# Kernel optimization log

Hardware: AMD Instinct MI355X
Metric: run time of the kernel (lower is better)

The kernel has to match this reference:

```python
import jax, jax.numpy as jnp
import numpy as np

B, N, D, H, F = 16, 512, 768, 12, 3072
HD = D // H
EPS = 1e-5
NEG_INF = -1e30  # stand-in for -inf; softmax of all -inf rows handled via nan_to_num semantics


def layer_norm(x, g, b):
    mu = jnp.mean(x, axis=-1, keepdims=True)
    var = jnp.mean(jnp.square(x - mu), axis=-1, keepdims=True)
    return (x - mu) * jax.lax.rsqrt(var + EPS) * g + b


def setup_inputs() -> dict:
    key = jax.random.key(0)
    ks = jax.random.split(key, 16)
    s = 0.02
    return {
        "x": jax.random.normal(ks[0], (B, N, D), jnp.float32),
        "spatial_encoding": jax.random.normal(ks[1], (B, N, N), jnp.float32),
        "edge_encoding": jax.random.normal(ks[2], (B, N, N), jnp.float32),
        "Wq": jax.random.normal(ks[3], (D, D), jnp.float32) * s,
        "Wk": jax.random.normal(ks[4], (D, D), jnp.float32) * s,
        "Wv": jax.random.normal(ks[5], (D, D), jnp.float32) * s,
        "bv": jnp.zeros((D,), jnp.float32),
        "Wo": jax.random.normal(ks[6], (D, D), jnp.float32) * s,
        "bo": jnp.zeros((D,), jnp.float32),
        "g1": jnp.ones((D,), jnp.float32),
        "be1": jnp.zeros((D,), jnp.float32),
        "g2": jnp.ones((D,), jnp.float32),
        "be2": jnp.zeros((D,), jnp.float32),
        "W1": jax.random.normal(ks[7], (D, F), jnp.float32) * s,
        "bf1": jnp.zeros((F,), jnp.float32),
        "W2": jax.random.normal(ks[8], (F, D), jnp.float32) * s,
        "bf2": jnp.zeros((D,), jnp.float32),
    }


def reference(x, spatial_encoding, edge_encoding, Wq, Wk, Wv, bv, Wo, bo,
              g1, be1, g2, be2, W1, bf1, W2, bf2):
    scale = D ** (-0.5)
    h = layer_norm(x, g1, be1)                              # n1(x)
    bias = (spatial_encoding + edge_encoding)[:, None]      # [B,1,N,N]

    q = (h @ Wq).reshape(B, N, H, HD).transpose(0, 2, 1, 3)  # [B,H,N,hd]
    k = (h @ Wk).reshape(B, N, H, HD).transpose(0, 2, 1, 3)
    v = (h @ Wv + bv).reshape(B, N, H, HD).transpose(0, 2, 1, 3)

    a = jnp.einsum('bhqd,bhkd->bhqk', q, k) * scale + bias   # [B,H,N,N]
    # pad rows (all-zero score rows) get -inf -> softmax NaN -> nan_to_num -> 0
    row_nonzero = jnp.any(a != 0, axis=-1, keepdims=True)
    a = jnp.where(row_nonzero, a, NEG_INF)
    p = jax.nn.softmax(a, axis=-1)
    p = jnp.where(row_nonzero, p, 0.0)  # mirrors nan_to_num on all -inf rows

    o = jnp.einsum('bhqk,bhkd->bhqd', p, v)                  # [B,H,N,hd]
    o = o.transpose(0, 2, 1, 3).reshape(B, N, D)
    att_output = o @ Wo + bo + x                              # residual

    pad_mask = jnp.any(att_output == 0, axis=-1)              # [B,N]
    ffn_in = layer_norm(x, g2, be2)                           # note: n2(x), as in source
    hmid = jax.nn.gelu(ffn_in @ W1 + bf1, approximate=True)
    ffn_out = hmid @ W2 + bf2 + att_output
    return jnp.where(pad_mask[..., None], 0.0, ffn_out)
```

## Files before the change

kernel.cpp:

```cpp
#include <hip/hip_runtime.h>
#include <math.h>

typedef unsigned short u16;
typedef __bf16 bf16x8 __attribute__((ext_vector_type(8)));
typedef float f32x4 __attribute__((ext_vector_type(4)));

__device__ __forceinline__ u16 f2bf(float f){
  union{float f; unsigned u;} v; v.f = f;
  return (u16)((v.u + 0x7fffu + ((v.u >> 16) & 1u)) >> 16);
}

#define LOG2E 1.4426950408889634f

__global__ __launch_bounds__(256) void prep_all(
    const float* __restrict__ sp, const float* __restrict__ ed,
    const float* __restrict__ Wq, const float* __restrict__ Wk,
    const float* __restrict__ Wv, const float* __restrict__ Wo,
    const float* __restrict__ W1, const float* __restrict__ W2,
    const float* __restrict__ g1, const float* __restrict__ g2,
    const float* __restrict__ be1, const float* __restrict__ be2,
    const float* __restrict__ bv, const float* __restrict__ bf1,
    const float* __restrict__ bo, const float* __restrict__ bf2,
    const float* __restrict__ x,
    u16* __restrict__ biasPb, u16* __restrict__ WqkvT, u16* __restrict__ WoT,
    u16* __restrict__ W1T, u16* __restrict__ W2T,
    float* __restrict__ qkvb, float* __restrict__ bf1f, float* __restrict__ bo2,
    u16* __restrict__ hn, float qscale){
  __shared__ float t[32][33];
  __shared__ float red[4][64];
  const int gbid = blockIdx.x, tid = threadIdx.x;

  if (gbid < 4096){
    int tt = gbid * 256 + tid;
    int row = tt >> 7, c0 = (tt & 127) * 4;
    size_t base = (size_t)row * 512;
    float4 s = *(const float4*)&sp[base + c0];
    float4 e = *(const float4*)&ed[base + c0];
    int kt = c0 >> 7, cw = c0 & 127, fk = cw >> 4, l0 = cw & 15;
    u16* o = biasPb + base + kt*128 + fk;
    o[(l0+0)*8] = f2bf((s.x+e.x)*LOG2E);
    o[(l0+1)*8] = f2bf((s.y+e.y)*LOG2E);
    o[(l0+2)*8] = f2bf((s.z+e.z)*LOG2E);
    o[(l0+3)*8] = f2bf((s.w+e.w)*LOG2E);
  } else if (gbid < 11008){
    int bid = gbid - 4096;
    const float* src; u16* dst; const float* rs; float sc; int R, C, bx, by;
    if (bid < 576)      {            src=Wq; dst=WqkvT;          rs=g1;      sc=qscale; R=768;  C=768;  bx=bid%24; by=bid/24; }
    else if (bid <1152) { bid-=576;  src=Wk; dst=WqkvT+768*768;  rs=g1;      sc=1.f;    R=768;  C=768;  bx=bid%24; by=bid/24; }
    else if (bid <1728) { bid-=1152; src=Wv; dst=WqkvT+1536*768; rs=g1;      sc=1.f;    R=768;  C=768;  bx=bid%24; by=bid/24; }
    else if (bid <2304) { bid-=1728; src=Wo; dst=WoT;            rs=nullptr; sc=1.f;    R=768;  C=768;  bx=bid%24; by=bid/24; }
    else if (bid <4608) { bid-=2304; src=W1; dst=W1T;            rs=g2;      sc=1.f;    R=768;  C=3072; bx=bid%96; by=bid/96; }
    else                { bid-=4608; src=W2; dst=W2T;            rs=nullptr; sc=1.f;    R=3072; C=768;  bx=bid%24; by=bid/24; }
    int c0 = bx * 32, r0 = by * 32;
    int tx = tid & 31, ty = tid >> 5;
    #pragma unroll
    for (int i = 0; i < 4; i++)
      t[ty + i*8][tx] = src[(size_t)(r0 + ty + i*8) * C + c0 + tx];
    __syncthreads();
    float fac = (rs ? rs[r0 + tx] : 1.f) * sc;
    #pragma unroll
    for (int i = 0; i < 4; i++)
      dst[(size_t)(c0 + ty + i*8) * R + r0 + tx] = f2bf(t[tx][ty + i*8] * fac);
  } else if (gbid < 11104){
    int fbid = gbid - 11008;
    int tx = tid & 63, ty = tid >> 6;
    int j = fbid * 64 + tx;
    if (j < 5376){
      const float* W; int col, stride; const float* bvec;
      if (j < 768)       { W = Wq; col = j;        stride = 768;  bvec = be1; }
      else if (j < 1536) { W = Wk; col = j - 768;  stride = 768;  bvec = be1; }
      else if (j < 2304) { W = Wv; col = j - 1536; stride = 768;  bvec = be1; }
      else               { W = W1; col = j - 2304; stride = 3072; bvec = be2; }
      float s = 0.f;
      for (int k = ty * 192; k < (ty + 1) * 192; k++)
        s += bvec[k] * W[(size_t)k * stride + col];
      red[ty][tx] = s;
    }
    __syncthreads();
    if (ty == 0){
      if (j < 5376){
        float s = red[0][tx] + red[1][tx] + red[2][tx] + red[3][tx];
        if (j < 1536)      qkvb[j] = s;
        else if (j < 2304) qkvb[j] = s + bv[j - 1536];
        else               bf1f[j - 2304] = s + bf1[j - 2304];
      } else {
        int col = j - 5376;
        bo2[col] = bo[col] + bf2[col];
      }
    }
  } else {
    int lbid = gbid - 11104;
    const int lane = tid & 63, wave = tid >> 6;
    const int row = lbid * 4 + wave;
    const float4* xr = (const float4*)(x + (size_t)row * 768);
    float4 v[3];
    float sum = 0.f, sq = 0.f;
    #pragma unroll
    for (int c = 0; c < 3; c++){
      v[c] = xr[lane + 64*c];
      sum += v[c].x + v[c].y + v[c].z + v[c].w;
      sq  += v[c].x*v[c].x + v[c].y*v[c].y + v[c].z*v[c].z + v[c].w*v[c].w;
    }
    #pragma unroll
    for (int d = 1; d < 64; d <<= 1){ sum += __shfl_xor(sum, d); sq += __shfl_xor(sq, d); }
    float mu  = sum * (1.f/768.f);
    float var = sq * (1.f/768.f) - mu*mu;
    float rs  = rsqrtf(var + 1e-5f);
    #pragma unroll
    for (int c = 0; c < 3; c++){
      int f4 = lane + 64*c;
      ushort4 o{f2bf((v[c].x-mu)*rs), f2bf((v[c].y-mu)*rs),
                f2bf((v[c].z-mu)*rs), f2bf((v[c].w-mu)*rs)};
      ((ushort4*)(hn + (size_t)row*768))[f4] = o;
    }
  }
}

__global__ __launch_bounds__(256, 2) void gemm_qkv(
    const u16* __restrict__ A, const u16* __restrict__ Bt, u16* __restrict__ Cout,
    const float* __restrict__ bias, u16* __restrict__ vt){
  const int Nn = 2304, K = 768;
  __shared__ __align__(16) u16 As[128*64];
  __shared__ __align__(16) u16 Bs[128*64];
  const int tid = threadIdx.x, lane = tid & 63, wave = tid >> 6;
  const int wm = wave >> 1, wn = wave & 1;
  const int l15 = lane & 15, lg = lane >> 4;
  const int bid = blockIdx.y * gridDim.x + blockIdx.x;
  const int cpx = (gridDim.x * gridDim.y) >> 3;
  const int swz = (bid & 7) * cpx + (bid >> 3);
  const int m0 = (swz / gridDim.x) * 128, n0 = (swz % gridDim.x) * 128;
  f32x4 acc[4][4] = {};
  for (int k0 = 0; k0 < K; k0 += 64){
    #pragma unroll
    for (int i = 0; i < 4; i++){
      int chunk = i*256 + tid;
      int row = chunk >> 3, seg = (chunk & 7) ^ (row & 7);
      __builtin_amdgcn_global_load_lds(
        (const __attribute__((address_space(1))) void*)&A[(size_t)(m0+row)*K + k0 + seg*8],
        (__attribute__((address_space(3))) void*)&As[(size_t)(i*256 + wave*64)*8], 16, 0, 0);
      __builtin_amdgcn_global_load_lds(
        (const __attribute__((address_space(1))) void*)&Bt[(size_t)(n0+row)*K + k0 + seg*8],
        (__attribute__((address_space(3))) void*)&Bs[(size_t)(i*256 + wave*64)*8], 16, 0, 0);
    }
    __syncthreads();
    bf16x8 af[4][2], bfr[4][2];
    #pragma unroll
    for (int i = 0; i < 4; i++){
      int ra = wm*64 + i*16 + l15, rb = wn*64 + i*16 + l15;
      #pragma unroll
      for (int kk = 0; kk < 2; kk++){
        af[i][kk]  = *(const bf16x8*)&As[ra*64 + (((kk*4 + lg) ^ (l15 & 7)) << 3)];
        bfr[i][kk] = *(const bf16x8*)&Bs[rb*64 + (((kk*4 + lg) ^ (l15 & 7)) << 3)];
      }
    }
    #pragma unroll
    for (int kk = 0; kk < 2; kk++)
      #pragma unroll
      for (int i = 0; i < 4; i++)
        #pragma unroll
        for (int j = 0; j < 4; j++)
          acc[i][j] = __builtin_amdgcn_mfma_f32_16x16x32_bf16(af[i][kk], bfr[j][kk], acc[i][j], 0, 0, 0);
    __syncthreads();
  }
  #pragma unroll
  for (int i = 0; i < 4; i++){
    int row_base = m0 + wm*64 + i*16 + lg*4;
    #pragma unroll
    for (int j = 0; j < 4; j++){
      int col = n0 + wn*64 + j*16 + l15;
      float bcol = bias[col];
      if (col >= 1536){
        int hv = (col - 1536) >> 6, hd = (col - 1536) & 63;
        int b = row_base >> 9, n = row_base & 511;
        int within = n & 127;
        int newn = (n & ~127) + ((((within >> 3) ^ (hd & 7)) << 3)) + (within & 7);
        ushort4 ov{f2bf(acc[i][j][0] + bcol), f2bf(acc[i][j][1] + bcol),
                   f2bf(acc[i][j][2] + bcol), f2bf(acc[i][j][3] + bcol)};
        *(ushort4*)&vt[(((size_t)(b*12 + hv)*64 + hd) << 9) + newn] = ov;
      } else {
        #pragma unroll
        for (int r = 0; r < 4; r++)
          Cout[(size_t)(row_base + r) * Nn + col] = f2bf(acc[i][j][r] + bcol);
      }
    }
  }
}

__device__ __forceinline__ void attn_body(
    int t, u16* sm, const u16* __restrict__ qkv, const u16* __restrict__ VTg,
    const u16* __restrict__ biasPb, u16* __restrict__ Og){
  u16* Ks = sm;
  u16* Vs = sm + 8192;
  u16* Pl = sm + 16384;
  const int tid = threadIdx.x, lane = tid & 63, wave = tid >> 6;
  const int l15 = lane & 15, lg = lane >> 4;
  const int swz = (t & 7) * 96 + (t >> 3);
  const int bh = swz >> 2, b = bh / 12, h = bh % 12;
  const int q0 = (swz & 3) * 128 + wave * 32;
  const u16* Qb = qkv + (size_t)b * 512 * 2304 + h * 64;
  const u16* Kb = Qb + 768;
  const u16* Vbh = VTg + (size_t)bh * 64 * 512;
  u16* Pw = &Pl[wave * 32 * 136];

  bf16x8 qf[2][2];
  #pragma unroll
  for (int fm = 0; fm < 2; fm++)
    #pragma unroll
    for (int kk = 0; kk < 2; kk++)
      qf[fm][kk] = *(const bf16x8*)&Qb[(size_t)(q0 + fm*16 + l15)*2304 + kk*32 + lg*8];

  f32x4 O[2][4] = {};
  float lrow[2][4] = {};

  for (int kt = 0; kt < 4; kt++){
    const int k0 = kt * 128;
    bf16x8 bb[2][4];
    #pragma unroll
    for (int fm = 0; fm < 2; fm++)
      #pragma unroll
      for (int r = 0; r < 4; r++){
        int qrow = q0 + fm*16 + lg*4 + r;
        bb[fm][r] = *(const bf16x8*)&biasPb[((size_t)(b*512 + qrow)*4 + kt)*128 + l15*8];
      }
    #pragma unroll
    for (int i = 0; i < 4; i++){
      int chunk = i*256 + tid;
      int r = chunk >> 3, cc = chunk & 7;
      __builtin_amdgcn_global_load_lds(
        (const __attribute__((address_space(1))) void*)&Kb[(size_t)(k0 + r)*2304 + ((cc ^ (r & 7)) << 3)],
        (__attribute__((address_space(3))) void*)&Ks[(size_t)(i*256 + wave*64)*8],
        16, 0, 0);
    }
    #pragma unroll
    for (int i = 0; i < 4; i++){
      int chunk = i*256 + tid;
      int r = chunk >> 4, cc = chunk & 15;
      __builtin_amdgcn_global_load_lds(
        (const __attribute__((address_space(1))) void*)&Vbh[(size_t)r*512 + k0 + (cc << 3)],
        (__attribute__((address_space(3))) void*)&Vs[(size_t)(i*256 + wave*64)*8],
        16, 0, 0);
    }
    __syncthreads();

    f32x4 S[2][8] = {};
    #pragma unroll
    for (int fk = 0; fk < 8; fk++)
      #pragma unroll
      for (int kk = 0; kk < 2; kk++){
        int row = fk*16 + l15;
        bf16x8 kf = *(const bf16x8*)&Ks[row*64 + (((kk*4 + lg) ^ (l15 & 7)) << 3)];
        S[0][fk] = __builtin_amdgcn_mfma_f32_16x16x32_bf16(qf[0][kk], kf, S[0][fk], 0,0,0);
        S[1][fk] = __builtin_amdgcn_mfma_f32_16x16x32_bf16(qf[1][kk], kf, S[1][fk], 0,0,0);
      }
    #pragma unroll
    for (int fm = 0; fm < 2; fm++)
      #pragma unroll
      for (int r = 0; r < 4; r++){
        float rs = 0.f;
        #pragma unroll
        for (int fk = 0; fk < 8; fk++){
          float p = exp2f(S[fm][fk][r] + (float)bb[fm][r][fk]);
          S[fm][fk][r] = p;
          rs += p;
        }
        rs += __shfl_xor(rs, 1); rs += __shfl_xor(rs, 2);
        rs += __shfl_xor(rs, 4); rs += __shfl_xor(rs, 8);
        lrow[fm][r] += rs;
      }
    #pragma unroll
    for (int fm = 0; fm < 2; fm++)
      #pragma unroll
      for (int fk = 0; fk < 8; fk++)
        #pragma unroll
        for (int r = 0; r < 4; r++)
          Pw[(fm*16 + lg*4 + r)*136 + fk*16 + l15] = f2bf(S[fm][fk][r]);
    bf16x8 pf[2][4];
    #pragma unroll
    for (int fm = 0; fm < 2; fm++)
      #pragma unroll
      for (int kk = 0; kk < 4; kk++)
        pf[fm][kk] = *(const bf16x8*)&Pw[(fm*16 + l15)*136 + kk*32 + lg*8];
    #pragma unroll
    for (int fn = 0; fn < 4; fn++)
      #pragma unroll
      for (int kk = 0; kk < 4; kk++){
        int row = fn*16 + l15;
        bf16x8 vf = *(const bf16x8*)&Vs[row*128 + (((kk*4 + lg) ^ (l15 & 7)) << 3)];
        O[0][fn] = __builtin_amdgcn_mfma_f32_16x16x32_bf16(pf[0][kk], vf, O[0][fn], 0,0,0);
        O[1][fn] = __builtin_amdgcn_mfma_f32_16x16x32_bf16(pf[1][kk], vf, O[1][fn], 0,0,0);
      }
    __syncthreads();
  }
  #pragma unroll
  for (int fm = 0; fm < 2; fm++)
    #pragma unroll
    for (int r = 0; r < 4; r++){
      float inv = __builtin_amdgcn_rcpf(lrow[fm][r]);
      int qrow = q0 + fm*16 + lg*4 + r;
      #pragma unroll
      for (int fn = 0; fn < 4; fn++)
        Og[((size_t)b*512 + qrow)*768 + h*64 + fn*16 + l15] = f2bf(O[fm][fn][r] * inv);
    }
}

__device__ __forceinline__ void ffn1_body(
    int fid, u16* sm, const u16* __restrict__ A, const u16* __restrict__ Bt,
    u16* __restrict__ Cout, const float* __restrict__ bias){
  u16* As = sm;
  u16* Bs = sm + 8192;
  const int Nn = 3072, K = 768;
  const int tid = threadIdx.x, lane = tid & 63, wave = tid >> 6;
  const int wm = wave >> 1, wn = wave & 1;
  const int l15 = lane & 15, lg = lane >> 4;
  const int swz = (fid & 7) * 192 + (fid >> 3);
  const int m0 = (swz / 24) * 128, n0 = (swz % 24) * 128;
  f32x4 acc[4][4] = {};
  for (int k0 = 0; k0 < K; k0 += 64){
    #pragma unroll
    for (int i = 0; i < 4; i++){
      int chunk = i*256 + tid;
      int row = chunk >> 3, seg = (chunk & 7) ^ (row & 7);
      __builtin_amdgcn_global_load_lds(
        (const __attribute__((address_space(1))) void*)&A[(size_t)(m0+row)*K + k0 + seg*8],
        (__attribute__((address_space(3))) void*)&As[(size_t)(i*256 + wave*64)*8], 16, 0, 0);
      __builtin_amdgcn_global_load_lds(
        (const __attribute__((address_space(1))) void*)&Bt[(size_t)(n0+row)*K + k0 + seg*8],
        (__attribute__((address_space(3))) void*)&Bs[(size_t)(i*256 + wave*64)*8], 16, 0, 0);
    }
    __syncthreads();
    bf16x8 af[4][2], bfr[4][2];
    #pragma unroll
    for (int i = 0; i < 4; i++){
      int ra = wm*64 + i*16 + l15, rb = wn*64 + i*16 + l15;
      #pragma unroll
      for (int kk = 0; kk < 2; kk++){
        af[i][kk]  = *(const bf16x8*)&As[ra*64 + (((kk*4 + lg) ^ (l15 & 7)) << 3)];
        bfr[i][kk] = *(const bf16x8*)&Bs[rb*64 + (((kk*4 + lg) ^ (l15 & 7)) << 3)];
      }
    }
    #pragma unroll
    for (int kk = 0; kk < 2; kk++)
      #pragma unroll
      for (int i = 0; i < 4; i++)
        #pragma unroll
        for (int j = 0; j < 4; j++)
          acc[i][j] = __builtin_amdgcn_mfma_f32_16x16x32_bf16(af[i][kk], bfr[j][kk], acc[i][j], 0, 0, 0);
    __syncthreads();
  }
  #pragma unroll
  for (int i = 0; i < 4; i++){
    int row_base = m0 + wm*64 + i*16 + lg*4;
    #pragma unroll
    for (int j = 0; j < 4; j++){
      int col = n0 + wn*64 + j*16 + l15;
      float bcol = bias[col];
      #pragma unroll
      for (int r = 0; r < 4; r++){
        size_t idx = (size_t)(row_base + r) * Nn + col;
        float v = acc[i][j][r] + bcol;
        float u = v + 0.044715f * v * v * v;
        float e = exp2f(-2.3022182f * u);
        Cout[idx] = f2bf(v * __builtin_amdgcn_rcpf(1.f + e));
      }
    }
  }
}

__global__ __launch_bounds__(256, 2) void attn_ffn1(
    const u16* __restrict__ qkv, const u16* __restrict__ VTg,
    const u16* __restrict__ biasPb, u16* __restrict__ Og,
    const u16* __restrict__ hn, const u16* __restrict__ W1T,
    u16* __restrict__ Gg, const float* __restrict__ bf1f){
  __shared__ __align__(16) u16 sm[33792];
  const int bid = blockIdx.x;
  if (bid < 768) attn_body(bid, sm, qkv, VTg, biasPb, Og);
  else           ffn1_body(bid - 768, sm, hn, W1T, Gg, bf1f);
}

__global__ __launch_bounds__(256, 2) void gemm_fin(
    const u16* __restrict__ Gg, const u16* __restrict__ Og,
    const u16* __restrict__ W2T, const u16* __restrict__ WoT,
    float* __restrict__ Cout, const float* __restrict__ bo2,
    const float* __restrict__ x){
  const int Nn = 768;
  __shared__ __align__(16) u16 As[128*64];
  __shared__ __align__(16) u16 Bs[128*64];
  const int tid = threadIdx.x, lane = tid & 63, wave = tid >> 6;
  const int wm = wave >> 1, wn = wave & 1;
  const int l15 = lane & 15, lg = lane >> 4;
  const int bid = blockIdx.y * gridDim.x + blockIdx.x;
  const int cpx = (gridDim.x * gridDim.y) >> 3;
  const int swz = (bid & 7) * cpx + (bid >> 3);
  const int m0 = (swz / gridDim.x) * 128, n0 = (swz % gridDim.x) * 128;
  f32x4 acc[4][4] = {};
  for (int k0 = 0; k0 < 3840; k0 += 64){
    const u16* Ab; const u16* Bb; int str; int kk0;
    if (k0 < 3072){ Ab = Gg; Bb = W2T; str = 3072; kk0 = k0; }
    else          { Ab = Og; Bb = WoT; str = 768;  kk0 = k0 - 3072; }
    #pragma unroll
    for (int i = 0; i < 4; i++){
      int chunk = i*256 + tid;
      int row = chunk >> 3, seg = (chunk & 7) ^ (row & 7);
      __builtin_amdgcn_global_load_lds(
        (const __attribute__((address_space(1))) void*)&Ab[(size_t)(m0+row)*str + kk0 + seg*8],
        (__attribute__((address_space(3))) void*)&As[(size_t)(i*256 + wave*64)*8], 16, 0, 0);
      __builtin_amdgcn_global_load_lds(
        (const __attribute__((address_space(1))) void*)&Bb[(size_t)(n0+row)*str + kk0 + seg*8],
        (__attribute__((address_space(3))) void*)&Bs[(size_t)(i*256 + wave*64)*8], 16, 0, 0);
    }
    __syncthreads();
    bf16x8 af[4][2], bfr[4][2];
    #pragma unroll
    for (int i = 0; i < 4; i++){
      int ra = wm*64 + i*16 + l15, rb = wn*64 + i*16 + l15;
      #pragma unroll
      for (int kk = 0; kk < 2; kk++){
        af[i][kk]  = *(const bf16x8*)&As[ra*64 + (((kk*4 + lg) ^ (l15 & 7)) << 3)];
        bfr[i][kk] = *(const bf16x8*)&Bs[rb*64 + (((kk*4 + lg) ^ (l15 & 7)) << 3)];
      }
    }
    #pragma unroll
    for (int kk = 0; kk < 2; kk++)
      #pragma unroll
      for (int i = 0; i < 4; i++)
        #pragma unroll
        for (int j = 0; j < 4; j++)
          acc[i][j] = __builtin_amdgcn_mfma_f32_16x16x32_bf16(af[i][kk], bfr[j][kk], acc[i][j], 0, 0, 0);
    __syncthreads();
  }
  #pragma unroll
  for (int i = 0; i < 4; i++){
    int row_base = m0 + wm*64 + i*16 + lg*4;
    #pragma unroll
    for (int j = 0; j < 4; j++){
      int col = n0 + wn*64 + j*16 + l15;
      float bcol = bo2[col];
      #pragma unroll
      for (int r = 0; r < 4; r++){
        size_t idx = (size_t)(row_base + r) * Nn + col;
        Cout[idx] = acc[i][j][r] + bcol + x[idx];
      }
    }
  }
}

extern "C" void kernel_launch(void* const* d_in, const int* in_sizes, int n_in,
                              void* d_out, int out_size, void* d_ws, size_t ws_size,
                              hipStream_t stream){
  const float* x   = (const float*)d_in[0];
  const float* sp  = (const float*)d_in[1];
  const float* ed  = (const float*)d_in[2];
  const float* Wq  = (const float*)d_in[3];
  const float* Wk  = (const float*)d_in[4];
  const float* Wv  = (const float*)d_in[5];
  const float* bv  = (const float*)d_in[6];
  const float* Wo  = (const float*)d_in[7];
  const float* bo  = (const float*)d_in[8];
  const float* g1  = (const float*)d_in[9];
  const float* be1 = (const float*)d_in[10];
  const float* g2  = (const float*)d_in[11];
  const float* be2 = (const float*)d_in[12];
  const float* W1  = (const float*)d_in[13];
  const float* bf1 = (const float*)d_in[14];
  const float* W2  = (const float*)d_in[15];
  const float* bf2 = (const float*)d_in[16];

  char* w = (char*)d_ws;
  size_t off = 0;
  auto alloc = [&](size_t bytes)->void*{ void* p = w + off; off += (bytes + 255) & ~(size_t)255; return p; };
  u16*   Gg    = (u16*)  alloc(8192ull*3072*2);
  u16*   qkv   = (u16*)  alloc(8192ull*2304*2);
  u16*   VTg   = (u16*)  alloc(8192ull*768*2);
  u16*   hn    = (u16*)  alloc(8192ull*768*2);
  u16*   Og    = (u16*)  alloc(8192ull*768*2);
  u16*   biasPb= (u16*)  alloc(16ull*512*512*2);
  u16*   WqkvT = (u16*)  alloc(2304ull*768*2);
  u16*   WoT   = (u16*)  alloc(768ull*768*2);
  u16*   W1T   = (u16*)  alloc(3072ull*768*2);
  u16*   W2T   = (u16*)  alloc(768ull*3072*2);
  float* qkvb  = (float*)alloc(2304ull*4);
  float* bf1f  = (float*)alloc(3072ull*4);
  float* bo2   = (float*)alloc(768ull*4);

  const float qscale = 0.03608439182435161f * LOG2E;

  prep_all<<<13152, 256, 0, stream>>>(sp, ed, Wq, Wk, Wv, Wo, W1, W2, g1, g2,
                                      be1, be2, bv, bf1, bo, bf2, x,
                                      biasPb, WqkvT, WoT, W1T, W2T,
                                      qkvb, bf1f, bo2, hn, qscale);

  gemm_qkv<<<dim3(18,64),256,0,stream>>>(hn, WqkvT, qkv, qkvb, VTg);

  attn_ffn1<<<2304, 256, 0, stream>>>(qkv, VTg, biasPb, Og, hn, W1T, Gg, bf1f);

  gemm_fin<<<dim3(6,64),256,0,stream>>>(Gg, Og, W2T, WoT, (float*)d_out, bo2, x);
}
```

Baseline: 230.3 us.

## Store FFN hidden activations and W2 in FP8 and use FP8 MFMA for FFN2

The GELU output of FFN1 and the transposed W2 weight are now written as FP8 with an XOR-swizzled layout, and the FFN2 part of the final GEMM uses the fp8 16x16x32 MFMA on them. This halves the bytes for the large 8192x3072 intermediate and for the W2 operand, and uses the higher-throughput FP8 matrix path. The Wo part stays in BF16 in a separate loop. The cost is a larger numerical error from FP8 rounding of activations and weights with no scaling, which may exceed tolerance.

```diff
diff --git a/kernel.cpp b/kernel.cpp
--- a/kernel.cpp
+++ b/kernel.cpp
@@ -2,12 +2,16 @@
 #include <math.h>
 
 typedef unsigned short u16;
+typedef unsigned char u8;
 typedef __bf16 bf16x8 __attribute__((ext_vector_type(8)));
 typedef float f32x4 __attribute__((ext_vector_type(4)));
 
 __device__ __forceinline__ u16 f2bf(float f){
   union{float f; unsigned u;} v; v.f = f;
   return (u16)((v.u + 0x7fffu + ((v.u >> 16) & 1u)) >> 16);
+}
+__device__ __forceinline__ u8 f2fp8(float f){
+  return (u8)(__builtin_amdgcn_cvt_pk_fp8_f32(f, f, 0, false) & 0xff);
 }
 
 #define LOG2E 1.4426950408889634f
@@ -23,7 +27,7 @@
     const float* __restrict__ bo, const float* __restrict__ bf2,
     const float* __restrict__ x,
     u16* __restrict__ biasPb, u16* __restrict__ WqkvT, u16* __restrict__ WoT,
-    u16* __restrict__ W1T, u16* __restrict__ W2T,
+    u16* __restrict__ W1T, u8* __restrict__ W2T8,
     float* __restrict__ qkvb, float* __restrict__ bf1f, float* __restrict__ bo2,
     u16* __restrict__ hn, float qscale){
   __shared__ float t[32][33];
@@ -44,23 +48,32 @@
     o[(l0+3)*8] = f2bf((s.w+e.w)*LOG2E);
   } else if (gbid < 11008){
     int bid = gbid - 4096;
-    const float* src; u16* dst; const float* rs; float sc; int R, C, bx, by;
-    if (bid < 576)      {            src=Wq; dst=WqkvT;          rs=g1;      sc=qscale; R=768;  C=768;  bx=bid%24; by=bid/24; }
-    else if (bid <1152) { bid-=576;  src=Wk; dst=WqkvT+768*768;  rs=g1;      sc=1.f;    R=768;  C=768;  bx=bid%24; by=bid/24; }
-    else if (bid <1728) { bid-=1152; src=Wv; dst=WqkvT+1536*768; rs=g1;      sc=1.f;    R=768;  C=768;  bx=bid%24; by=bid/24; }
-    else if (bid <2304) { bid-=1728; src=Wo; dst=WoT;            rs=nullptr; sc=1.f;    R=768;  C=768;  bx=bid%24; by=bid/24; }
-    else if (bid <4608) { bid-=2304; src=W1; dst=W1T;            rs=g2;      sc=1.f;    R=768;  C=3072; bx=bid%96; by=bid/96; }
-    else                { bid-=4608; src=W2; dst=W2T;            rs=nullptr; sc=1.f;    R=3072; C=768;  bx=bid%24; by=bid/24; }
+    const float* src; u16* dst; const float* rs; float sc; int C, bx, by; bool w2 = false;
+    if (bid < 576)      {            src=Wq; dst=WqkvT;          rs=g1;      sc=qscale; C=768;  bx=bid%24; by=bid/24; }
+    else if (bid <1152) { bid-=576;  src=Wk; dst=WqkvT+768*768;  rs=g1;      sc=1.f;    C=768;  bx=bid%24; by=bid/24; }
+    else if (bid <1728) { bid-=1152; src=Wv; dst=WqkvT+1536*768; rs=g1;      sc=1.f;    C=768;  bx=bid%24; by=bid/24; }
+    else if (bid <2304) { bid-=1728; src=Wo; dst=WoT;            rs=nullptr; sc=1.f;    C=768;  bx=bid%24; by=bid/24; }
+    else if (bid <4608) { bid-=2304; src=W1; dst=W1T;            rs=g2;      sc=1.f;    C=3072; bx=bid%96; by=bid/96; }
+    else                { bid-=4608; src=W2; dst=nullptr;        rs=nullptr; sc=1.f;    C=768;  bx=bid%24; by=bid/24; w2 = true; }
     int c0 = bx * 32, r0 = by * 32;
     int tx = tid & 31, ty = tid >> 5;
     #pragma unroll
     for (int i = 0; i < 4; i++)
       t[ty + i*8][tx] = src[(size_t)(r0 + ty + i*8) * C + c0 + tx];
     __syncthreads();
-    float fac = (rs ? rs[r0 + tx] : 1.f) * sc;
-    #pragma unroll
-    for (int i = 0; i < 4; i++)
-      dst[(size_t)(c0 + ty + i*8) * R + r0 + tx] = f2bf(t[tx][ty + i*8] * fac);
+    if (w2){
+      #pragma unroll
+      for (int i = 0; i < 4; i++){
+        int n = c0 + ty + i*8, k = r0 + tx;
+        size_t a = (size_t)n*3072 + (k & ~63) + ((((k>>3)&7) ^ (n&7)) << 3) + (k&7);
+        W2T8[a] = f2fp8(t[tx][ty + i*8]);
+      }
+    } else {
+      float fac = (rs ? rs[r0 + tx] : 1.f) * sc;
+      #pragma unroll
+      for (int i = 0; i < 4; i++)
+        dst[(size_t)(c0 + ty + i*8) * 768 + r0 + tx] = f2bf(t[tx][ty + i*8] * fac);
+    }
   } else if (gbid < 11104){
     int fbid = gbid - 11008;
     int tx = tid & 63, ty = tid >> 6;
@@ -305,10 +318,10 @@
 
 __device__ __forceinline__ void ffn1_body(
     int fid, u16* sm, const u16* __restrict__ A, const u16* __restrict__ Bt,
-    u16* __restrict__ Cout, const float* __restrict__ bias){
+    u8* __restrict__ Cout, const float* __restrict__ bias){
   u16* As = sm;
   u16* Bs = sm + 8192;
-  const int Nn = 3072, K = 768;
+  const int K = 768;
   const int tid = threadIdx.x, lane = tid & 63, wave = tid >> 6;
   const int wm = wave >> 1, wn = wave & 1;
   const int l15 = lane & 15, lg = lane >> 4;
@@ -354,13 +367,15 @@
     for (int j = 0; j < 4; j++){
       int col = n0 + wn*64 + j*16 + l15;
       float bcol = bias[col];
+      int cbase = col & ~63, c8 = (col >> 3) & 7, c7 = col & 7;
       #pragma unroll
       for (int r = 0; r < 4; r++){
-        size_t idx = (size_t)(row_base + r) * Nn + col;
+        int row = row_base + r;
         float v = acc[i][j][r] + bcol;
         float u = v + 0.044715f * v * v * v;
         float e = exp2f(-2.3022182f * u);
-        Cout[idx] = f2bf(v * __builtin_amdgcn_rcpf(1.f + e));
+        float g = v * __builtin_amdgcn_rcpf(1.f + e);
+        Cout[(size_t)row*3072 + cbase + ((c8 ^ (row & 7)) << 3) + c7] = f2fp8(g);
       }
     }
   }
@@ -370,21 +385,23 @@
     const u16* __restrict__ qkv, const u16* __restrict__ VTg,
     const u16* __restrict__ biasPb, u16* __restrict__ Og,
     const u16* __restrict__ hn, const u16* __restrict__ W1T,
-    u16* __restrict__ Gg, const float* __restrict__ bf1f){
+    u8* __restrict__ Gg8, const float* __restrict__ bf1f){
   __shared__ __align__(16) u16 sm[33792];
   const int bid = blockIdx.x;
   if (bid < 768) attn_body(bid, sm, qkv, VTg, biasPb, Og);
-  else           ffn1_body(bid - 768, sm, hn, W1T, Gg, bf1f);
+  else           ffn1_body(bid - 768, sm, hn, W1T, Gg8, bf1f);
 }
 
 __global__ __launch_bounds__(256, 2) void gemm_fin(
-    const u16* __restrict__ Gg, const u16* __restrict__ Og,
-    const u16* __restrict__ W2T, const u16* __restrict__ WoT,
+    const u8* __restrict__ Gg8, const u16* __restrict__ Og,
+    const u8* __restrict__ W2T8, const u16* __restrict__ WoT,
     float* __restrict__ Cout, const float* __restrict__ bo2,
     const float* __restrict__ x){
   const int Nn = 768;
   __shared__ __align__(16) u16 As[128*64];
   __shared__ __align__(16) u16 Bs[128*64];
+  u8* As8 = (u8*)As;
+  u8* Bs8 = (u8*)Bs;
   const int tid = threadIdx.x, lane = tid & 63, wave = tid >> 6;
   const int wm = wave >> 1, wn = wave & 1;
   const int l15 = lane & 15, lg = lane >> 4;
@@ -393,19 +410,50 @@
   const int swz = (bid & 7) * cpx + (bid >> 3);
   const int m0 = (swz / gridDim.x) * 128, n0 = (swz % gridDim.x) * 128;
   f32x4 acc[4][4] = {};
-  for (int k0 = 0; k0 < 3840; k0 += 64){
-    const u16* Ab; const u16* Bb; int str; int kk0;
-    if (k0 < 3072){ Ab = Gg; Bb = W2T; str = 3072; kk0 = k0; }
-    else          { Ab = Og; Bb = WoT; str = 768;  kk0 = k0 - 3072; }
+
+  for (int k0 = 0; k0 < 3072; k0 += 64){
+    #pragma unroll
+    for (int i = 0; i < 2; i++){
+      int chunk = i*256 + tid;
+      int row = chunk >> 2, c16 = chunk & 3;
+      __builtin_amdgcn_global_load_lds(
+        (const __attribute__((address_space(1))) void*)&Gg8[(size_t)(m0+row)*3072 + k0 + c16*16],
+        (__attribute__((address_space(3))) void*)&As8[(size_t)(i*256 + wave*64)*16], 16, 0, 0);
+      __builtin_amdgcn_global_load_lds(
+        (const __attribute__((address_space(1))) void*)&W2T8[(size_t)(n0+row)*3072 + k0 + c16*16],
+        (__attribute__((address_space(3))) void*)&Bs8[(size_t)(i*256 + wave*64)*16], 16, 0, 0);
+    }
+    __syncthreads();
+    long a8[4][2], b8[4][2];
+    #pragma unroll
+    for (int i = 0; i < 4; i++){
+      int ra = wm*64 + i*16 + l15, rb = wn*64 + i*16 + l15;
+      #pragma unroll
+      for (int kk = 0; kk < 2; kk++){
+        a8[i][kk] = *(const long*)&As8[ra*64 + (((kk*4 + lg) ^ (l15 & 7)) << 3)];
+        b8[i][kk] = *(const long*)&Bs8[rb*64 + (((kk*4 + lg) ^ (l15 & 7)) << 3)];
+      }
+    }
+    #pragma unroll
+    for (int kk = 0; kk < 2; kk++)
+      #pragma unroll
+      for (int i = 0; i < 4; i++)
+        #pragma unroll
+        for (int j = 0; j < 4; j++)
+          acc[i][j] = __builtin_amdgcn_mfma_f32_16x16x32_fp8_fp8(a8[i][kk], b8[j][kk], acc[i][j], 0, 0, 0);
+    __syncthreads();
+  }
+
+  for (int k0 = 0; k0 < 768; k0 += 64){
     #pragma unroll
     for (int i = 0; i < 4; i++){
       int chunk = i*256 + tid;
       int row = chunk >> 3, seg = (chunk & 7) ^ (row & 7);
       __builtin_amdgcn_global_load_lds(
-        (const __attribute__((address_space(1))) void*)&Ab[(size_t)(m0+row)*str + kk0 + seg*8],
+        (const __attribute__((address_space(1))) void*)&Og[(size_t)(m0+row)*768 + k0 + seg*8],
         (__attribute__((address_space(3))) void*)&As[(size_t)(i*256 + wave*64)*8], 16, 0, 0);
       __builtin_amdgcn_global_load_lds(
-        (const __attribute__((address_space(1))) void*)&Bb[(size_t)(n0+row)*str + kk0 + seg*8],
+        (const __attribute__((address_space(1))) void*)&WoT[(size_t)(n0+row)*768 + k0 + seg*8],
         (__attribute__((address_space(3))) void*)&Bs[(size_t)(i*256 + wave*64)*8], 16, 0, 0);
     }
     __syncthreads();
@@ -428,6 +476,7 @@
           acc[i][j] = __builtin_amdgcn_mfma_f32_16x16x32_bf16(af[i][kk], bfr[j][kk], acc[i][j], 0, 0, 0);
     __syncthreads();
   }
+
   #pragma unroll
   for (int i = 0; i < 4; i++){
     int row_base = m0 + wm*64 + i*16 + lg*4;
@@ -468,7 +517,7 @@
   char* w = (char*)d_ws;
   size_t off = 0;
   auto alloc = [&](size_t bytes)->void*{ void* p = w + off; off += (bytes + 255) & ~(size_t)255; return p; };
-  u16*   Gg    = (u16*)  alloc(8192ull*3072*2);
+  u8*    Gg8   = (u8*)   alloc(8192ull*3072);
   u16*   qkv   = (u16*)  alloc(8192ull*2304*2);
   u16*   VTg   = (u16*)  alloc(8192ull*768*2);
   u16*   hn    = (u16*)  alloc(8192ull*768*2);
@@ -477,7 +526,7 @@
   u16*   WqkvT = (u16*)  alloc(2304ull*768*2);
   u16*   WoT   = (u16*)  alloc(768ull*768*2);
   u16*   W1T   = (u16*)  alloc(3072ull*768*2);
-  u16*   W2T   = (u16*)  alloc(768ull*3072*2);
+  u8*    W2T8  = (u8*)   alloc(768ull*3072);
   float* qkvb  = (float*)alloc(2304ull*4);
   float* bf1f  = (float*)alloc(3072ull*4);
   float* bo2   = (float*)alloc(768ull*4);
@@ -486,12 +535,12 @@
 
   prep_all<<<13152, 256, 0, stream>>>(sp, ed, Wq, Wk, Wv, Wo, W1, W2, g1, g2,
                                       be1, be2, bv, bf1, bo, bf2, x,
-                                      biasPb, WqkvT, WoT, W1T, W2T,
+                                      biasPb, WqkvT, WoT, W1T, W2T8,
                                       qkvb, bf1f, bo2, hn, qscale);
 
   gemm_qkv<<<dim3(18,64),256,0,stream>>>(hn, WqkvT, qkv, qkvb, VTg);
 
-  attn_ffn1<<<2304, 256, 0, stream>>>(qkv, VTg, biasPb, Og, hn, W1T, Gg, bf1f);
-
-  gemm_fin<<<dim3(6,64),256,0,stream>>>(Gg, Og, W2T, WoT, (float*)d_out, bo2, x);
-}
+  attn_ffn1<<<2304, 256, 0, stream>>>(qkv, VTg, biasPb, Og, hn, W1T, Gg8, bf1f);
+
+  gemm_fin<<<dim3(6,64),256,0,stream>>>(Gg8, Og, W2T8, WoT, (float*)d_out, bo2, x);
+}
```

Result: faster. 220.2 us (-4.4%).
